# Kernel optimization log

Measured on AMD Instinct MI355X. Metric: run time of the kernel, lower is better.

## Reference

```python
import jax, jax.numpy as jnp
import numpy as np

TOPK_FRAC = 0.05  # init arg `topk` (fraction of pool kept)


def setup_inputs() -> dict:
    key = jax.random.key(0)
    k1, k2 = jax.random.split(key)
    x = jax.random.normal(k1, (16, 256, 32, 32), dtype=jnp.float32)
    # nn.Parameter(torch.rand(P, C)) -> uniform [0, 1)
    visual_concept_pool = jax.random.uniform(k2, (2048, 256), dtype=jnp.float32)
    return {"x": x, "visual_concept_pool": visual_concept_pool}


def reference(x, visual_concept_pool):
    n, c, h, w = x.shape
    P = visual_concept_pool.shape[0]
    L = h * w
    xf = x.reshape(n, c, L)                              # [n, c, L]
    # dot_product[n, P, L] = pool @ xf
    dot = jnp.einsum('pc,ncl->npl', visual_concept_pool, xf)
    pool_norm = jnp.sqrt(jnp.sum(visual_concept_pool ** 2, axis=1))   # [P]
    x_norm = jnp.sqrt(jnp.sum(xf ** 2, axis=1))                        # [n, L]
    cos = dot / (pool_norm[None, :, None] * x_norm[:, None, :])       # [n, P, L]

    # mode 1.1: top-k over the pool dimension per (n, pixel)
    keep = int(TOPK_FRAC * P)
    cos_t = jnp.transpose(cos, (0, 2, 1))                # [n, L, P]
    _, idx = jax.lax.top_k(jnp.abs(cos_t), keep)         # [n, L, keep]
    mask = jnp.zeros_like(cos_t).at[
        jnp.arange(n)[:, None, None],
        jnp.arange(L)[None, :, None],
        idx,
    ].set(1.0)                                           # [n, L, P]
    masked = cos_t * mask
    normed = masked / jnp.sum(masked, axis=-1, keepdims=True)  # renormalize over P
    # reconstruct[n, c, L] = pool^T @ cos
    recon = jnp.einsum('pc,nlp->ncl', visual_concept_pool, normed)
    return recon.reshape(n, c, h, w)
```

## Files before the change

kernel.cpp:

```cpp
#include <hip/hip_runtime.h>
#include <hip/hip_fp16.h>

typedef unsigned short u16;
typedef _Float16 half8 __attribute__((ext_vector_type(8)));
typedef float floatx4 __attribute__((ext_vector_type(4)));

#define C_DIM 256
#define P_DIM 2048
#define L_DIM 1024
#define N_DIM 16
#define KEEP 102
#define KPAD 104
#define QTR_PIX 4096
#define SCALE 256.0f

__device__ __forceinline__ void st8(u16* dst, const u16* s) {
  uint4 u;
  u.x = (unsigned)s[0] | ((unsigned)s[1] << 16);
  u.y = (unsigned)s[2] | ((unsigned)s[3] << 16);
  u.z = (unsigned)s[4] | ((unsigned)s[5] << 16);
  u.w = (unsigned)s[6] | ((unsigned)s[7] << 16);
  *(uint4*)dst = u;
}

__device__ __forceinline__ u16 f2h_ftz(float v) {
  if (fabsf(v) < 6.103515625e-5f) return 0;
  return __half_as_ushort(__float2half(v));
}

__device__ __forceinline__ void gl_lds16(const u16* g, u16* l) {
  __builtin_amdgcn_global_load_lds(
      (const __attribute__((address_space(1))) unsigned int*)g,
      (__attribute__((address_space(3))) unsigned int*)l, 16, 0, 0);
}

union SMem {
  u16 sB[2][2][8][512];
  struct { float tbuf[8][260]; int2 kpw[8][KPAD]; } sel;
};

__global__ __launch_bounds__(256) void k_pinv(const float* __restrict__ pool,
                                              float* __restrict__ pinv) {
  int p = blockIdx.x * 256 + threadIdx.x;
  const float4* row = (const float4*)(pool + (size_t)p * C_DIM);
  float s = 0.f;
#pragma unroll
  for (int i = 0; i < C_DIM / 4; ++i) {
    float4 v = row[i];
    s += v.x * v.x + v.y * v.y + v.z * v.z + v.w * v.w;
  }
  pinv[p] = 1.0f / sqrtf(s);
}

__device__ __forceinline__ void packpool_body(int b,
                                              const float* __restrict__ pool,
                                              const float* __restrict__ pinv,
                                              u16* __restrict__ ah,
                                              u16* __restrict__ al,
                                              u16* __restrict__ ph) {
  int tid = b * 512 + threadIdx.x;
  int lane = tid & 63;
  int ks = (tid >> 6) & 7;
  int pm = tid >> 9;
  int p = pm * 16 + (lane & 15);
  int c0 = ks * 32 + ((lane >> 4) << 3);
  float sc = pinv[p] * SCALE;
  const float* src = pool + (size_t)p * C_DIM + c0;
  u16 h8[8], l8[8], p8[8];
#pragma unroll
  for (int j = 0; j < 8; ++j) {
    float raw = src[j];
    p8[j] = __half_as_ushort(__float2half(raw));
    float v = raw * sc;
    u16 h = f2h_ftz(v);
    float r = v - __half2float(__ushort_as_half(h));
    h8[j] = h;
    l8[j] = f2h_ftz(r);
  }
  size_t o = (size_t)tid * 8;
  st8(ah + o, h8); st8(al + o, l8);
  st8(ph + (size_t)p * C_DIM + c0, p8);
}

__device__ __forceinline__ void packx_body(int pb, int pq,
                                           const float* __restrict__ x,
                                           u16* __restrict__ xh,
                                           u16* __restrict__ xl) {
  int t = threadIdx.x;
  int lane = t & 63;
  int ks = (t >> 6) & 7;
  int pn = pq * 256 + pb;
  int pix = pn * 16 + (lane & 15);
  int n = pix >> 10, l = pix & 1023;
  int c0 = ks * 32 + ((lane >> 4) << 3);
  const float* src = x + ((size_t)(n * C_DIM + c0)) * L_DIM + l;
  u16 h8[8], l8[8];
#pragma unroll
  for (int j = 0; j < 8; ++j) {
    float v = src[(size_t)j * L_DIM] * SCALE;
    u16 h = f2h_ftz(v);
    float r = v - __half2float(__ushort_as_half(h));
    h8[j] = h;
    l8[j] = f2h_ftz(r);
  }
  size_t o = ((size_t)pn * 512 + (size_t)ks * 64 + lane) * 8;
  st8(xh + o, h8); st8(xl + o, l8);
}

__global__ __launch_bounds__(512) void k_pre(const float* __restrict__ pool,
                                             const float* __restrict__ pinv,
                                             u16* __restrict__ ah,
                                             u16* __restrict__ al,
                                             u16* __restrict__ ph,
                                             const float* __restrict__ x,
                                             u16* __restrict__ xh,
                                             u16* __restrict__ xl) {
  int b = blockIdx.x;
  if (b < 128) packpool_body(b, pool, pinv, ah, al, ph);
  else packx_body(b - 128, 0, x, xh, xl);
}

__device__ __forceinline__ void mfma_body(int b, int mq,
                                          const u16* __restrict__ ah_,
                                          const u16* __restrict__ al_,
                                          const u16* __restrict__ xh_,
                                          const u16* __restrict__ xl_,
                                          float* __restrict__ sbuf,
                                          u16 (*sB)[2][8][512]) {
  const int t = threadIdx.x, lane = t & 63, w = t >> 6;
  const int pT = b & 15, pixT = b >> 4;
  const int pm = pT * 8 + w;
  const int pnBase = mq * 256 + pixT * 8;
  const half8* A8h = (const half8*)ah_;
  const half8* A8l = (const half8*)al_;
  const u16* xsrc[2] = {xh_, xl_};

  floatx4 acc[8];
#pragma unroll
  for (int nt = 0; nt < 8; ++nt) acc[nt] = (floatx4){0.f, 0.f, 0.f, 0.f};

#pragma unroll
  for (int q = 0; q < 2; ++q) {
    int id = w * 2 + q;
    int arr = id >> 3, nt = id & 7;
    gl_lds16(xsrc[arr] + ((size_t)(pnBase + nt) * 512 + lane) * 8,
             &sB[0][arr][nt][0]);
  }
  __syncthreads();

#pragma unroll 1
  for (int ks = 0; ks < 8; ++ks) {
    const int cur = ks & 1;
    half8 aH, aL;
    {
      size_t idx = (size_t)pm * 512 + (size_t)ks * 64 + lane;
      aH = A8h[idx]; aL = A8l[idx];
    }
    if (ks < 7) {
#pragma unroll
      for (int q = 0; q < 2; ++q) {
        int id = w * 2 + q;
        int arr = id >> 3, nt = id & 7;
        gl_lds16(xsrc[arr] + ((size_t)(pnBase + nt) * 512 + (ks + 1) * 64 + lane) * 8,
                 &sB[cur ^ 1][arr][nt][0]);
      }
    }
#pragma unroll
    for (int nt = 0; nt < 8; ++nt) {
      half8 bh = *(const half8*)&sB[cur][0][nt][lane * 8];
      half8 bl = *(const half8*)&sB[cur][1][nt][lane * 8];
      floatx4 c = acc[nt];
      c = __builtin_amdgcn_mfma_f32_16x16x32_f16(aH, bh, c, 0, 0, 0);
      c = __builtin_amdgcn_mfma_f32_16x16x32_f16(aH, bl, c, 0, 0, 0);
      c = __builtin_amdgcn_mfma_f32_16x16x32_f16(aL, bh, c, 0, 0, 0);
      acc[nt] = c;
    }
    __syncthreads();
  }

  const int qr = lane >> 4, cl = lane & 15;
  const int pix0 = pixT * 128;
  const int pcol = pT * 128 + w * 16;
#pragma unroll
  for (int nt = 0; nt < 8; ++nt) {
    float* dst = sbuf + (size_t)(pix0 + nt * 16 + cl) * P_DIM + pcol + qr * 4;
    *(float4*)dst = make_float4(acc[nt][0], acc[nt][1], acc[nt][2], acc[nt][3]);
  }
}

__device__ __forceinline__ void select_body(int b, int sq,
                                            const float* __restrict__ sbuf,
                                            const u16* __restrict__ pool_h,
                                            float* __restrict__ out,
                                            float (*tbuf)[260],
                                            int2 (*kpw)[KPAD]) {
  const int t = threadIdx.x;
  const int lane = t & 63;
  const int wv = t >> 6;
  const int gp0 = sq * QTR_PIX + b * 8;
  const int n = gp0 >> 10;
  const int l0 = gp0 & 1023;
  const float* sp = sbuf + (size_t)(b * 8 + wv) * P_DIM;

  float4 v[8];
#pragma unroll
  for (int q = 0; q < 8; ++q) v[q] = *(const float4*)(sp + q * 256 + lane * 4);

  if (lane < KPAD - KEEP) kpw[wv][KEEP + lane] = make_int2(0, 0);

  float M = 0.f;
#pragma unroll
  for (int q = 0; q < 8; ++q) {
    M = fmaxf(M, fabsf(v[q].x)); M = fmaxf(M, fabsf(v[q].y));
    M = fmaxf(M, fabsf(v[q].z)); M = fmaxf(M, fabsf(v[q].w));
  }
#pragma unroll
  for (int off = 1; off < 64; off <<= 1) M = fmaxf(M, __shfl_xor(M, off));
  const unsigned bitsM = __float_as_uint(M);

  unsigned lo = 0u, hi = bitsM + 1u;
  unsigned cl = 2048u, ch = 0u;
  bool exact = false;
  unsigned m = (bitsM > (5u << 23)) ? (bitsM - (5u << 23)) : ((lo + hi) >> 1);
  int it = 0;
  while (hi - lo > 1u) {
    float mf = __uint_as_float(m);
    unsigned cnt = 0;
#pragma unroll
    for (int q = 0; q < 8; ++q) {
      cnt += (unsigned)__popcll(__ballot(fabsf(v[q].x) >= mf));
      cnt += (unsigned)__popcll(__ballot(fabsf(v[q].y) >= mf));
      cnt += (unsigned)__popcll(__ballot(fabsf(v[q].z) >= mf));
      cnt += (unsigned)__popcll(__ballot(fabsf(v[q].w) >= mf));
    }
    if (cnt == (unsigned)KEEP) { lo = m; exact = true; break; }
    if (cnt > (unsigned)KEEP) { lo = m; cl = cnt; } else { hi = m; ch = cnt; }
    unsigned span = hi - lo;
    if (span <= 1u) break;
    unsigned step;
    if ((++it & 1) != 0) {
      step = (unsigned)((float)span * (float)(cl - KEEP) / (float)(cl - ch));
    } else {
      step = span >> 1;
    }
    if (step < 1u) step = 1u;
    else if (step > span - 1u) step = span - 1u;
    m = lo + step;
  }
  const float V = __uint_as_float(lo);
  const float Vp = exact ? V : __uint_as_float(lo + 1u);

  unsigned rrem = 0u;
  if (!exact) {
    unsigned gt = 0;
#pragma unroll
    for (int q = 0; q < 8; ++q) {
      gt += (unsigned)__popcll(__ballot(fabsf(v[q].x) >= Vp));
      gt += (unsigned)__popcll(__ballot(fabsf(v[q].y) >= Vp));
      gt += (unsigned)__popcll(__ballot(fabsf(v[q].z) >= Vp));
      gt += (unsigned)__popcll(__ballot(fabsf(v[q].w) >= Vp));
    }
    rrem = (unsigned)KEEP - gt;
  }

  unsigned gmask[8], tmask[8];
#pragma unroll
  for (int q = 0; q < 8; ++q) {
    const float* f = (const float*)&v[q];
    unsigned gm = 0, tm = 0;
#pragma unroll
    for (int rr = 0; rr < 4; ++rr) {
      float av = fabsf(f[rr]);
      if (av >= Vp) gm |= (1u << rr);
      else if (av >= V) tm |= (1u << rr);
    }
    gmask[q] = gm; tmask[q] = tm;
  }

  const unsigned long long lowm = (1ull << lane) - 1ull;
  unsigned base = 0, tiebase = 0;
  float Ssum = 0.f;
#pragma unroll
  for (int q = 0; q < 8; ++q) {
    const float* f = (const float*)&v[q];
    unsigned km = gmask[q];
    if (rrem != 0u) {
      unsigned teq = 0, myeqb = 0;
#pragma unroll
      for (int rr = 0; rr < 4; ++rr) {
        unsigned long long beq = __ballot((tmask[q] >> rr) & 1u);
        teq += (unsigned)__popcll(beq);
        myeqb += (unsigned)__popcll(beq & lowm);
      }
      unsigned cum = 0;
#pragma unroll
      for (int rr = 0; rr < 4; ++rr) {
        if ((tmask[q] >> rr) & 1u) {
          if (tiebase + myeqb + cum < rrem) km |= (1u << rr);
          ++cum;
        }
      }
      tiebase += teq;
    }
    unsigned long long bk[4];
    unsigned tot = 0, myb = 0;
#pragma unroll
    for (int rr = 0; rr < 4; ++rr) {
      bk[rr] = __ballot((km >> rr) & 1u);
      tot += (unsigned)__popcll(bk[rr]);
      myb += (unsigned)__popcll(bk[rr] & lowm);
    }
    {
      unsigned cum = 0;
#pragma unroll
      for (int rr = 0; rr < 4; ++rr) {
        if ((km >> rr) & 1u) {
          unsigned pos = base + myb + cum;
          kpw[wv][pos] = make_int2(q * 256 + lane * 4 + rr, __float_as_int(f[rr]));
          Ssum += f[rr];
          ++cum;
        }
      }
    }
    base += tot;
  }

#pragma unroll
  for (int off = 1; off < 64; off <<= 1) Ssum += __shfl_xor(Ssum, off);
  const float invS = 1.0f / Ssum;

  __builtin_amdgcn_wave_barrier();

  float a0 = 0.f, a1 = 0.f, a2 = 0.f, a3 = 0.f;
  const u16* pb = pool_h + 4 * lane;
  int2 e[4];
  uint2 r[4];
#pragma unroll
  for (int j = 0; j < 4; ++j) e[j] = kpw[wv][j];
#pragma unroll
  for (int j = 0; j < 4; ++j) r[j] = *(const uint2*)(pb + (size_t)e[j].x * C_DIM);
  for (int k = 0; k < KPAD; k += 4) {
    int kn = (k + 4 < KPAD) ? k + 4 : 0;
    int2 en[4];
    uint2 rn[4];
#pragma unroll
    for (int j = 0; j < 4; ++j) en[j] = kpw[wv][kn + j];
#pragma unroll
    for (int j = 0; j < 4; ++j) rn[j] = *(const uint2*)(pb + (size_t)en[j].x * C_DIM);
#pragma unroll
    for (int j = 0; j < 4; ++j) {
      float w2 = __int_as_float(e[j].y);
      unsigned rx = r[j].x, ry = r[j].y;
      asm volatile("v_fma_mix_f32 %0, %1, %2, %0 op_sel:[0,0,0] op_sel_hi:[0,1,0]"
                   : "+v"(a0) : "v"(w2), "v"(rx));
      asm volatile("v_fma_mix_f32 %0, %1, %2, %0 op_sel:[0,1,0] op_sel_hi:[0,1,0]"
                   : "+v"(a1) : "v"(w2), "v"(rx));
      asm volatile("v_fma_mix_f32 %0, %1, %2, %0 op_sel:[0,0,0] op_sel_hi:[0,1,0]"
                   : "+v"(a2) : "v"(w2), "v"(ry));
      asm volatile("v_fma_mix_f32 %0, %1, %2, %0 op_sel:[0,1,0] op_sel_hi:[0,1,0]"
                   : "+v"(a3) : "v"(w2), "v"(ry));
    }
#pragma unroll
    for (int j = 0; j < 4; ++j) { e[j] = en[j]; r[j] = rn[j]; }
  }
  a0 *= invS; a1 *= invS; a2 *= invS; a3 *= invS;

  *(float4*)&tbuf[wv][4 * lane] = make_float4(a0, a1, a2, a3);
  __syncthreads();

  {
    int c = t >> 1, lq = t & 1;
    float4 o = make_float4(tbuf[4 * lq + 0][c], tbuf[4 * lq + 1][c],
                           tbuf[4 * lq + 2][c], tbuf[4 * lq + 3][c]);
    *(float4*)(out + ((size_t)(n * C_DIM + c)) * L_DIM + l0 + 4 * lq) = o;
  }
}

__global__ __launch_bounds__(512, 4) void k_main(const u16* __restrict__ ah_,
                                                 const u16* __restrict__ al_,
                                                 const u16* __restrict__ xh_,
                                                 const u16* __restrict__ xl_,
                                                 const u16* __restrict__ ph,
                                                 const float* __restrict__ x,
                                                 float* __restrict__ sbuf0,
                                                 float* __restrict__ sbuf1,
                                                 float* __restrict__ out,
                                                 int mq, int sq, int pq) {
  __shared__ __align__(16) SMem sm;
  const int b = blockIdx.x;
  const int nsel = (sq >= 0) ? 512 : 0;
  const int npk = (pq >= 0) ? 256 : 0;
  if (b < nsel) {
    select_body(b, sq, (sq & 1) ? sbuf1 : sbuf0, ph, out, sm.sel.tbuf, sm.sel.kpw);
  } else if (b < nsel + npk) {
    packx_body(b - nsel, pq, x, (u16*)xh_, (u16*)xl_);
  } else {
    mfma_body(b - nsel - npk, mq, ah_, al_, xh_, xl_, (mq & 1) ? sbuf1 : sbuf0, sm.sB);
  }
}

extern "C" void kernel_launch(void* const* d_in, const int* in_sizes, int n_in,
                              void* d_out, int out_size, void* d_ws, size_t ws_size,
                              hipStream_t stream) {
  const float* x = (const float*)d_in[0];
  const float* pool = (const float*)d_in[1];
  float* out = (float*)d_out;
  char* wsb = (char*)d_ws;
  float* sbuf0 = (float*)wsb;
  float* sbuf1 = (float*)(wsb + 33554432);
  u16* xh = (u16*)(wsb + 67108864);
  u16* xl = xh + 4194304;
  u16* ah = xl + 4194304;
  u16* al = ah + 524288;
  u16* ph = al + 524288;
  float* pinv = (float*)(ph + 524288);

  k_pinv<<<P_DIM / 256, 256, 0, stream>>>(pool, pinv);
  k_pre<<<384, 512, 0, stream>>>(pool, pinv, ah, al, ph, x, xh, xl);

  k_main<<<768, 512, 0, stream>>>(ah, al, xh, xl, ph, x, sbuf0, sbuf1, out, 0, -1, 1);
  k_main<<<1280, 512, 0, stream>>>(ah, al, xh, xl, ph, x, sbuf0, sbuf1, out, 1, 0, 2);
  k_main<<<1280, 512, 0, stream>>>(ah, al, xh, xl, ph, x, sbuf0, sbuf1, out, 2, 1, 3);
  k_main<<<1024, 512, 0, stream>>>(ah, al, xh, xl, ph, x, sbuf0, sbuf1, out, 3, 2, -1);
  k_main<<<512, 512, 0, stream>>>(ah, al, xh, xl, ph, x, sbuf0, sbuf1, out, -1, 3, -1);
}
```

Baseline: 252.7 us.

## Batch four threshold probes in top-k select and ping-pong pool gathers

Before the iterative search, the top-k threshold search now tests four exponent-offset guesses in a single pass over the register values, which narrows the bracket with fewer serial ballot rounds. The selected indices are stored pre-scaled to byte offsets (index<<9), so the gather needs no multiply. The reconstruction loop is restructured into an A/B ping-pong over groups of four entries, with the next group's loads issued before the current group's FMAs. The cost is extra ballots on the first pass and more live registers.

```diff
diff --git a/kernel.cpp b/kernel.cpp
--- a/kernel.cpp
+++ b/kernel.cpp
@@ -218,13 +218,7 @@
   for (int off = 1; off < 64; off <<= 1) M = fmaxf(M, __shfl_xor(M, off));
   const unsigned bitsM = __float_as_uint(M);
 
-  unsigned lo = 0u, hi = bitsM + 1u;
-  unsigned cl = 2048u, ch = 0u;
-  bool exact = false;
-  unsigned m = (bitsM > (5u << 23)) ? (bitsM - (5u << 23)) : ((lo + hi) >> 1);
-  int it = 0;
-  while (hi - lo > 1u) {
-    float mf = __uint_as_float(m);
+  auto countGE = [&](float mf) -> unsigned {
     unsigned cnt = 0;
 #pragma unroll
     for (int q = 0; q < 8; ++q) {
@@ -233,33 +227,63 @@
       cnt += (unsigned)__popcll(__ballot(fabsf(v[q].z) >= mf));
       cnt += (unsigned)__popcll(__ballot(fabsf(v[q].w) >= mf));
     }
-    if (cnt == (unsigned)KEEP) { lo = m; exact = true; break; }
-    if (cnt > (unsigned)KEEP) { lo = m; cl = cnt; } else { hi = m; ch = cnt; }
+    return cnt;
+  };
+
+  const unsigned t1 = (bitsM > (1u << 23)) ? bitsM - (1u << 23) : 1u;
+  const unsigned t2 = (bitsM > (2u << 23)) ? bitsM - (2u << 23) : 1u;
+  const unsigned t3 = (bitsM > (3u << 23)) ? bitsM - (3u << 23) : 1u;
+  const unsigned t4 = (bitsM > (5u << 23)) ? bitsM - (5u << 23) : 1u;
+  const float g1 = __uint_as_float(t1), g2 = __uint_as_float(t2);
+  const float g3 = __uint_as_float(t3), g4 = __uint_as_float(t4);
+  unsigned c1 = 0, c2 = 0, c3 = 0, c4 = 0;
+#pragma unroll
+  for (int q = 0; q < 8; ++q) {
+    const float* f = (const float*)&v[q];
+#pragma unroll
+    for (int rr = 0; rr < 4; ++rr) {
+      float av = fabsf(f[rr]);
+      c1 += (unsigned)__popcll(__ballot(av >= g1));
+      c2 += (unsigned)__popcll(__ballot(av >= g2));
+      c3 += (unsigned)__popcll(__ballot(av >= g3));
+      c4 += (unsigned)__popcll(__ballot(av >= g4));
+    }
+  }
+
+  unsigned lo = 0u, hi = 1u, cl_ = P_DIM, ch_ = 0u;
+  bool exact = false;
+  if (c1 == (unsigned)KEEP)      { lo = t1; exact = true; }
+  else if (c2 == (unsigned)KEEP) { lo = t2; exact = true; }
+  else if (c3 == (unsigned)KEEP) { lo = t3; exact = true; }
+  else if (c4 == (unsigned)KEEP) { lo = t4; exact = true; }
+  else if (c1 > (unsigned)KEEP)  { lo = t1; cl_ = c1; hi = bitsM + 1u; ch_ = 0u; }
+  else if (c2 > (unsigned)KEEP)  { lo = t2; cl_ = c2; hi = t1; ch_ = c1; }
+  else if (c3 > (unsigned)KEEP)  { lo = t3; cl_ = c3; hi = t2; ch_ = c2; }
+  else if (c4 > (unsigned)KEEP)  { lo = t4; cl_ = c4; hi = t3; ch_ = c3; }
+  else                           { lo = 0u; cl_ = P_DIM; hi = t4; ch_ = c4; }
+
+  int it = 0;
+  while (!exact && hi - lo > 1u) {
     unsigned span = hi - lo;
-    if (span <= 1u) break;
     unsigned step;
-    if ((++it & 1) != 0) {
-      step = (unsigned)((float)span * (float)(cl - KEEP) / (float)(cl - ch));
+    if ((it++ & 1) == 0) {
+      step = (unsigned)((float)span * (float)(cl_ - KEEP) / (float)(cl_ - ch_));
     } else {
       step = span >> 1;
     }
     if (step < 1u) step = 1u;
     else if (step > span - 1u) step = span - 1u;
-    m = lo + step;
+    unsigned m = lo + step;
+    unsigned cnt = countGE(__uint_as_float(m));
+    if (cnt == (unsigned)KEEP) { lo = m; exact = true; break; }
+    if (cnt > (unsigned)KEEP) { lo = m; cl_ = cnt; } else { hi = m; ch_ = cnt; }
   }
   const float V = __uint_as_float(lo);
   const float Vp = exact ? V : __uint_as_float(lo + 1u);
 
   unsigned rrem = 0u;
   if (!exact) {
-    unsigned gt = 0;
-#pragma unroll
-    for (int q = 0; q < 8; ++q) {
-      gt += (unsigned)__popcll(__ballot(fabsf(v[q].x) >= Vp));
-      gt += (unsigned)__popcll(__ballot(fabsf(v[q].y) >= Vp));
-      gt += (unsigned)__popcll(__ballot(fabsf(v[q].z) >= Vp));
-      gt += (unsigned)__popcll(__ballot(fabsf(v[q].w) >= Vp));
-    }
+    unsigned gt = countGE(Vp);
     rrem = (unsigned)KEEP - gt;
   }
 
@@ -316,7 +340,8 @@
       for (int rr = 0; rr < 4; ++rr) {
         if ((km >> rr) & 1u) {
           unsigned pos = base + myb + cum;
-          kpw[wv][pos] = make_int2(q * 256 + lane * 4 + rr, __float_as_int(f[rr]));
+          kpw[wv][pos] = make_int2((q * 256 + lane * 4 + rr) << 9,
+                                   __float_as_int(f[rr]));
           Ssum += f[rr];
           ++cum;
         }
@@ -332,21 +357,11 @@
   __builtin_amdgcn_wave_barrier();
 
   float a0 = 0.f, a1 = 0.f, a2 = 0.f, a3 = 0.f;
-  const u16* pb = pool_h + 4 * lane;
-  int2 e[4];
-  uint2 r[4];
-#pragma unroll
-  for (int j = 0; j < 4; ++j) e[j] = kpw[wv][j];
-#pragma unroll
-  for (int j = 0; j < 4; ++j) r[j] = *(const uint2*)(pb + (size_t)e[j].x * C_DIM);
-  for (int k = 0; k < KPAD; k += 4) {
-    int kn = (k + 4 < KPAD) ? k + 4 : 0;
-    int2 en[4];
-    uint2 rn[4];
-#pragma unroll
-    for (int j = 0; j < 4; ++j) en[j] = kpw[wv][kn + j];
-#pragma unroll
-    for (int j = 0; j < 4; ++j) rn[j] = *(const uint2*)(pb + (size_t)en[j].x * C_DIM);
+  const char* pb = (const char*)(pool_h + 4 * lane);
+  int2 eA[4], eB[4];
+  uint2 rA[4], rB[4];
+
+  auto PROC = [&](const int2* e, const uint2* r) {
 #pragma unroll
     for (int j = 0; j < 4; ++j) {
       float w2 = __int_as_float(e[j].y);
@@ -360,8 +375,30 @@
       asm volatile("v_fma_mix_f32 %0, %1, %2, %0 op_sel:[0,1,0] op_sel_hi:[0,1,0]"
                    : "+v"(a3) : "v"(w2), "v"(ry));
     }
-#pragma unroll
-    for (int j = 0; j < 4; ++j) { e[j] = en[j]; r[j] = rn[j]; }
+  };
+
+#pragma unroll
+  for (int j = 0; j < 4; ++j) eA[j] = kpw[wv][j];
+#pragma unroll
+  for (int j = 0; j < 4; ++j)
+    rA[j] = *(const uint2*)(pb + (unsigned)eA[j].x);
+
+#pragma unroll 1
+  for (int k = 0; k < KPAD; k += 8) {
+    const int kb = k + 4;
+#pragma unroll
+    for (int j = 0; j < 4; ++j) eB[j] = kpw[wv][kb + j];
+#pragma unroll
+    for (int j = 0; j < 4; ++j)
+      rB[j] = *(const uint2*)(pb + (unsigned)eB[j].x);
+    PROC(eA, rA);
+    const int ka = (k + 8 < KPAD) ? k + 8 : 0;
+#pragma unroll
+    for (int j = 0; j < 4; ++j) eA[j] = kpw[wv][ka + j];
+#pragma unroll
+    for (int j = 0; j < 4; ++j)
+      rA[j] = *(const uint2*)(pb + (unsigned)eA[j].x);
+    PROC(eB, rB);
   }
   a0 *= invS; a1 *= invS; a2 *= invS; a3 *= invS;
 
```

Result: no change. 249.1 us (-1.5%).
